# Kernel optimization log

Hardware: AMD Instinct MI355X
Metric: run time of the kernel (lower is better)

Reference implementation:

```python
import jax, jax.numpy as jnp
import numpy as np

B, C, H, W = 16, 512, 32, 32
HID = 4 * C


def setup_inputs() -> dict:
    key = jax.random.key(0)
    k_x, k_w1, k_w2 = jax.random.split(key, 3)
    x = jax.random.normal(k_x, (B, C, H, W), dtype=jnp.float32)
    # 1x1 conv weights stored as [out, in] matrices (kernel_size=1)
    w1 = jax.random.normal(k_w1, (HID, C), dtype=jnp.float32) * (1.0 / np.sqrt(C))
    b1 = jnp.zeros((HID,), dtype=jnp.float32)
    w2 = jax.random.normal(k_w2, (C, HID), dtype=jnp.float32) * (1.0 / np.sqrt(HID))
    b2 = jnp.zeros((C,), dtype=jnp.float32)
    return {"x": x, "w1": w1, "b1": b1, "w2": w2, "b2": b2}


def reference(x, w1, b1, w2, b2):
    Bd, Cd, Hd, Wd = x.shape
    scale = Cd ** (-0.5)
    xf = x.reshape(Bd, Cd, Hd * Wd)          # [B, C, N]
    q = jnp.swapaxes(xf, -1, -2)              # [B, N, C]
    # full spatial self-attention: scores [B, N, N]
    attn = jax.nn.softmax(jnp.einsum('bnc,bcm->bnm', q, xf) * scale, axis=-1)
    out = jnp.einsum('bnm,bmc->bnc', attn, q)  # [B, N, C]
    # 1x1-conv FFN applied per spatial position
    h = jax.nn.relu(jnp.einsum('bnc,dc->bnd', out, w1) + b1)   # [B, N, 4C]
    y = jnp.einsum('bnd,cd->bnc', h, w2) + b2                  # [B, N, C]
    y = jnp.swapaxes(y, -1, -2).reshape(Bd, Cd, Hd, Wd)
    return y + x
```

## Files before the change

kernel.cpp:

```cpp
#include <hip/hip_runtime.h>

#define BATCH 16
#define CH    512
#define NSP   1024
#define HIDD  2048

typedef __bf16 bf16x8 __attribute__((ext_vector_type(8)));
typedef float floatx4 __attribute__((ext_vector_type(4)));

__device__ __forceinline__ float bf2f(unsigned short u) {
    union { unsigned int i; float f; } v; v.i = ((unsigned int)u) << 16; return v.f;
}
__device__ __forceinline__ unsigned short f2bf(float f) {
    union { float f; unsigned int i; } v; v.f = f;
    unsigned int i = v.i;
    return (unsigned short)((i + 0x7FFFu + ((i >> 16) & 1u)) >> 16);
}

__device__ __forceinline__ void gload16(const void* g, void* l) {
    __builtin_amdgcn_global_load_lds(
        (__attribute__((address_space(1))) unsigned int*)(g),
        (__attribute__((address_space(3))) unsigned int*)(l),
        16, 0, 0);
}
#define MEMFENCE asm volatile("" ::: "memory")

template<int EPI, int MAP, int DEPTH>
__global__ __launch_bounds__(256, (DEPTH == 2) ? 3 : 2)
void gemm_bt(const unsigned short* __restrict__ A,
             const unsigned short* __restrict__ Bm,
             void* __restrict__ Cout,
             int Nn, int K,
             long sAb, long sBb, long sCb,
             const float* __restrict__ bias, float scale,
             const float* __restrict__ resid,
             float* __restrict__ aux)
{
    constexpr int NBUF = DEPTH + 1;
    __shared__ unsigned short sA[NBUF][128 * 32];
    __shared__ unsigned short sB[NBUF][128 * 32];
    __shared__ float sInv[128];

    const int tid  = threadIdx.x;
    const int lane = tid & 63;
    const int w    = tid >> 6;
    const int quad = lane >> 4;
    const int l15  = lane & 15;
    const int mw   = (w >> 1) * 64;
    const int nw   = (w & 1) * 64;

    const int F = blockIdx.x;
    int m0, n0, b;
    if constexpr (MAP == 1) {
        const int xcd = F & 7, s = F >> 3;
        b = xcd + ((s >> 5) << 3);
        const int j = s & 31; m0 = (j >> 2) << 7; n0 = (j & 3) << 7;
    } else if constexpr (MAP == 3) {
        const int xcd = F & 7, s = F >> 3;
        b = 0; m0 = (s & 3) << 7; n0 = ((xcd << 4) + (s >> 2)) << 7;
    } else {
        const int xcd = F & 7; int s = F >> 3;
        b = xcd + ((s >= 36) ? 8 : 0);
        if (s >= 36) s -= 36;
        int tm = 0;
        while (s >= 8 - tm) { s -= 8 - tm; tm++; }
        m0 = tm << 7; n0 = (tm + s) << 7;
    }

    if constexpr (EPI == 6) {
        if (tid < 128) {
            const float* p = aux + (size_t)b * NSP * 16
                           + (size_t)(m0 + tid) * 16;
            float s = 0.f;
#pragma unroll
            for (int k = 0; k < 16; k++) s += p[k];
            sInv[tid] = 1.0f / s;
        }
        MEMFENCE;
    }

    A  += (size_t)b * sAb;
    Bm += (size_t)b * sBb;

    const int srow = lane >> 2;
    const int sg   = (lane & 3) ^ ((lane >> 3) & 3);
    const unsigned short* pA = A  + (size_t)(m0 + w * 32 + srow) * K + sg * 8;
    const unsigned short* pB = Bm + (size_t)(n0 + w * 32 + srow) * K + sg * 8;
    const size_t rowskip16 = (size_t)16 * K;
    const int woff = w * 1024;
    const int rslot = ((l15 >> 1) & 3);

    floatx4 acc[4][4];
#pragma unroll
    for (int i = 0; i < 4; i++)
#pragma unroll
        for (int j = 0; j < 4; j++) acc[i][j] = (floatx4){0.f, 0.f, 0.f, 0.f};

    const int nIter = K >> 5;
    const int kLast = K - 32;

#pragma unroll
    for (int d = 0; d < DEPTH; ++d) {
        unsigned short* dA = &sA[d][0] + woff;
        unsigned short* dB = &sB[d][0] + woff;
        gload16(pA + d * 32,             dA);
        gload16(pA + d * 32 + rowskip16, dA + 512);
        gload16(pB + d * 32,             dB);
        gload16(pB + d * 32 + rowskip16, dB + 512);
        MEMFENCE;
    }

    int bcur = 0, bpf = DEPTH;
    for (int it = 0; it < nIter; ++it) {
        if constexpr (DEPTH == 2)
            asm volatile("s_waitcnt vmcnt(4)\n\ts_barrier" ::: "memory");
        else
            asm volatile("s_waitcnt vmcnt(8)\n\ts_barrier" ::: "memory");

        const int kpf = (it + DEPTH) * 32 <= kLast ? (it + DEPTH) * 32 : kLast;
        unsigned short* dA = &sA[0][0] + bpf * 4096 + woff;
        unsigned short* dB = &sB[0][0] + bpf * 4096 + woff;
        gload16(pA + kpf,             dA);
        gload16(pA + kpf + rowskip16, dA + 512);
        gload16(pB + kpf,             dB);
        gload16(pB + kpf + rowskip16, dB + 512);
        MEMFENCE;

        const unsigned short* bufA = &sA[0][0] + bcur * 4096;
        const unsigned short* bufB = &sB[0][0] + bcur * 4096;
        bf16x8 af[4], bfr[4];
#pragma unroll
        for (int mi = 0; mi < 4; mi++)
            af[mi] = *(const bf16x8*)(bufA + (mw + mi * 16 + l15) * 32
                                      + (quad ^ rslot) * 8);
#pragma unroll
        for (int ni = 0; ni < 4; ni++)
            bfr[ni] = *(const bf16x8*)(bufB + (nw + ni * 16 + l15) * 32
                                       + (quad ^ rslot) * 8);
#pragma unroll
        for (int mi = 0; mi < 4; mi++)
#pragma unroll
            for (int ni = 0; ni < 4; ni++)
                acc[mi][ni] = __builtin_amdgcn_mfma_f32_16x16x32_bf16(
                    af[mi], bfr[ni], acc[mi][ni], 0, 0, 0);

        bcur = bcur == NBUF - 1 ? 0 : bcur + 1;
        bpf  = bpf  == NBUF - 1 ? 0 : bpf  + 1;
    }
    asm volatile("s_waitcnt vmcnt(0)" ::: "memory");

    if constexpr (EPI == 4) {
        float* Of = (float*)Cout;
#pragma unroll
        for (int mi = 0; mi < 4; mi++) {
#pragma unroll
            for (int r = 0; r < 4; r++) {
                const int c = m0 + mw + mi * 16 + quad * 4 + r;
                const float bv = bias[c];
#pragma unroll
                for (int ni = 0; ni < 4; ni++) {
                    const int j  = n0 + nw + ni * 16 + l15;
                    const int bb = j >> 10, ns = j & 1023;
                    const size_t a = (size_t)bb * CH * NSP + (size_t)c * NSP + ns;
                    Of[a] = acc[mi][ni][r] + bv + resid[a];
                }
            }
        }
    } else if constexpr (EPI == 5) {
#pragma unroll
        for (int mi = 0; mi < 4; mi++)
#pragma unroll
            for (int ni = 0; ni < 4; ni++)
#pragma unroll
                for (int r = 0; r < 4; r++)
                    acc[mi][ni][r] = __expf(acc[mi][ni][r] * scale);
        {
            const int chunk = (n0 + nw) >> 6;
            float* ps = aux + (size_t)b * NSP * 16;
#pragma unroll
            for (int mi = 0; mi < 4; mi++) {
#pragma unroll
                for (int r = 0; r < 4; r++) {
                    float s = acc[mi][0][r] + acc[mi][1][r]
                            + acc[mi][2][r] + acc[mi][3][r];
                    s += __shfl_xor(s, 1);
                    s += __shfl_xor(s, 2);
                    s += __shfl_xor(s, 4);
                    s += __shfl_xor(s, 8);
                    if (l15 == 0)
                        ps[(size_t)(m0 + mw + mi * 16 + quad * 4 + r) * 16
                           + chunk] = s;
                }
            }
        }
        unsigned short* Cb = (unsigned short*)Cout + (size_t)b * sCb;
#pragma unroll
        for (int mi = 0; mi < 4; mi++) {
#pragma unroll
            for (int r = 0; r < 4; r++) {
                const size_t rowoff =
                    (size_t)(m0 + mw + mi * 16 + quad * 4 + r) * Nn;
#pragma unroll
                for (int ni = 0; ni < 4; ni++)
                    Cb[rowoff + n0 + nw + ni * 16 + l15] =
                        f2bf(acc[mi][ni][r]);
            }
        }
        if constexpr (MAP == 4) {
            if (m0 != n0) {
                const int chunkt = (m0 + mw) >> 6;
                float* ps = aux + (size_t)b * NSP * 16;
#pragma unroll
                for (int ni = 0; ni < 4; ni++) {
                    float s = 0.f;
#pragma unroll
                    for (int mi = 0; mi < 4; mi++)
#pragma unroll
                        for (int r = 0; r < 4; r++) s += acc[mi][ni][r];
                    s += __shfl_xor(s, 16);
                    s += __shfl_xor(s, 32);
                    if (quad == 0)
                        ps[(size_t)(n0 + nw + ni * 16 + l15) * 16 + chunkt] = s;
                }
#pragma unroll
                for (int ni = 0; ni < 4; ni++) {
                    const size_t rowoff =
                        (size_t)(n0 + nw + ni * 16 + l15) * Nn;
#pragma unroll
                    for (int mi = 0; mi < 4; mi++) {
                        ushort4 v;
                        v.x = f2bf(acc[mi][ni][0]);
                        v.y = f2bf(acc[mi][ni][1]);
                        v.z = f2bf(acc[mi][ni][2]);
                        v.w = f2bf(acc[mi][ni][3]);
                        *(ushort4*)(Cb + rowoff + m0 + mw + mi * 16 + quad * 4)
                            = v;
                    }
                }
            }
        }
    } else {
        __syncthreads();
        unsigned short* Cb = (unsigned short*)Cout + (size_t)b * sCb;
#pragma unroll
        for (int mi = 0; mi < 4; mi++) {
#pragma unroll
            for (int r = 0; r < 4; r++) {
                const int lrow = mw + mi * 16 + quad * 4 + r;
                const float iv = sInv[lrow];
                const size_t rowoff = (size_t)(m0 + lrow) * Nn;
#pragma unroll
                for (int ni = 0; ni < 4; ni++)
                    Cb[rowoff + n0 + nw + ni * 16 + l15] =
                        f2bf(acc[mi][ni][r] * iv);
            }
        }
    }
}

__global__ __launch_bounds__(256, 2)
void gemm_final_u2(const unsigned short* __restrict__ A,
                   const unsigned short* __restrict__ Bm,
                   float* __restrict__ Of,
                   const float* __restrict__ bias,
                   const float* __restrict__ resid)
{
    const int K = HIDD;
    __shared__ unsigned short sA[4][128 * 32];
    __shared__ unsigned short sB[4][128 * 32];

    const int tid  = threadIdx.x;
    const int lane = tid & 63;
    const int w    = tid >> 6;
    const int quad = lane >> 4;
    const int l15  = lane & 15;
    const int mw   = (w >> 1) * 64;
    const int nw   = (w & 1) * 64;

    const int F = blockIdx.x;
    const int xcd = F & 7, s = F >> 3;
    const int m0 = (s & 3) << 7;
    const int n0 = ((xcd << 4) + (s >> 2)) << 7;

    const int srow = lane >> 2;
    const int sg   = (lane & 3) ^ ((lane >> 3) & 3);
    const unsigned short* pA = A  + (size_t)(m0 + w * 32 + srow) * K + sg * 8;
    const unsigned short* pB = Bm + (size_t)(n0 + w * 32 + srow) * K + sg * 8;
    const size_t rowskip16 = (size_t)16 * K;
    const int woff = w * 1024;
    const int rslot = ((l15 >> 1) & 3);

    floatx4 acc[4][4];
#pragma unroll
    for (int i = 0; i < 4; i++)
#pragma unroll
        for (int j = 0; j < 4; j++) acc[i][j] = (floatx4){0.f, 0.f, 0.f, 0.f};

    const int kLast = K - 32;

#pragma unroll
    for (int d = 0; d < 4; ++d) {
        unsigned short* dA = &sA[d][0] + woff;
        unsigned short* dB = &sB[d][0] + woff;
        gload16(pA + d * 32,             dA);
        gload16(pA + d * 32 + rowskip16, dA + 512);
        gload16(pB + d * 32,             dB);
        gload16(pB + d * 32 + rowskip16, dB + 512);
        MEMFENCE;
    }

    const int nBody = K >> 6;
    for (int i = 0; i < nBody; ++i) {
        asm volatile("s_waitcnt vmcnt(8)\n\ts_barrier" ::: "memory");

#pragma unroll
        for (int t = 0; t < 2; ++t) {
            const int buf = (2 * i + t) & 3;
            const unsigned short* bufA = &sA[buf][0];
            const unsigned short* bufB = &sB[buf][0];
            bf16x8 af[4], bfr[4];
#pragma unroll
            for (int mi = 0; mi < 4; mi++)
                af[mi] = *(const bf16x8*)(bufA + (mw + mi * 16 + l15) * 32
                                          + (quad ^ rslot) * 8);
#pragma unroll
            for (int ni = 0; ni < 4; ni++)
                bfr[ni] = *(const bf16x8*)(bufB + (nw + ni * 16 + l15) * 32
                                           + (quad ^ rslot) * 8);
#pragma unroll
            for (int mi = 0; mi < 4; mi++)
#pragma unroll
                for (int ni = 0; ni < 4; ni++)
                    acc[mi][ni] = __builtin_amdgcn_mfma_f32_16x16x32_bf16(
                        af[mi], bfr[ni], acc[mi][ni], 0, 0, 0);
        }

        __builtin_amdgcn_s_barrier();
#pragma unroll
        for (int t = 0; t < 2; ++t) {
            const int kt = 2 * i + 4 + t;
            const int kpf = (kt * 32 <= kLast) ? kt * 32 : kLast;
            const int buf = kt & 3;
            unsigned short* dA = &sA[buf][0] + woff;
            unsigned short* dB = &sB[buf][0] + woff;
            gload16(pA + kpf,             dA);
            gload16(pA + kpf + rowskip16, dA + 512);
            gload16(pB + kpf,             dB);
            gload16(pB + kpf + rowskip16, dB + 512);
            MEMFENCE;
        }
    }
    asm volatile("s_waitcnt vmcnt(0)" ::: "memory");

#pragma unroll
    for (int mi = 0; mi < 4; mi++) {
#pragma unroll
        for (int r = 0; r < 4; r++) {
            const int c = m0 + mw + mi * 16 + quad * 4 + r;
            const float bv = bias[c];
#pragma unroll
            for (int ni = 0; ni < 4; ni++) {
                const int j  = n0 + nw + ni * 16 + l15;
                const int bb = j >> 10, ns = j & 1023;
                const size_t a = (size_t)bb * CH * NSP + (size_t)c * NSP + ns;
                Of[a] = acc[mi][ni][r] + bv + resid[a];
            }
        }
    }
}

__global__ __launch_bounds__(256, 3)
void ffn1_wide(const unsigned short* __restrict__ A,
               const unsigned short* __restrict__ Bm,
               unsigned short* __restrict__ Cout,
               const float* __restrict__ bias)
{
    const int K = CH, Nn = HIDD;
    __shared__ unsigned short sA[2][128 * 32];
    __shared__ unsigned short sB[2][256 * 32];

    const int tid  = threadIdx.x;
    const int lane = tid & 63;
    const int w    = tid >> 6;
    const int quad = lane >> 4;
    const int l15  = lane & 15;
    const int mw   = (w >> 1) * 64;
    const int nw   = (w & 1) * 128;

    const int F = blockIdx.x;
    const int xcd = F & 7, s = F >> 3;
    const int m0 = ((xcd << 4) + (s >> 3)) << 7;
    const int n0 = (s & 7) << 8;

    const int srow = lane >> 2;
    const int sg   = (lane & 3) ^ ((lane >> 3) & 3);
    const unsigned short* pA = A  + (size_t)(m0 + w * 32 + srow) * K + sg * 8;
    const unsigned short* pB = Bm + (size_t)(n0 + w * 64 + srow) * K + sg * 8;
    const size_t rowskip16 = (size_t)16 * K;
    const int woffA = w * 1024;
    const int woffB = w * 2048;
    const int rslot = ((l15 >> 1) & 3);

    floatx4 acc[4][8];
#pragma unroll
    for (int i = 0; i < 4; i++)
#pragma unroll
        for (int j = 0; j < 8; j++) acc[i][j] = (floatx4){0.f, 0.f, 0.f, 0.f};

    const int nIter = K >> 5;
    const int kLast = K - 32;

#pragma unroll
    for (int d = 0; d < 2; ++d) {
        unsigned short* dA = &sA[d][0] + woffA;
        unsigned short* dB = &sB[d][0] + woffB;
        gload16(pA + d * 32,                 dA);
        gload16(pA + d * 32 +     rowskip16, dA + 512);
        gload16(pB + d * 32,                 dB);
        gload16(pB + d * 32 +     rowskip16, dB + 512);
        gload16(pB + d * 32 + 2 * rowskip16, dB + 1024);
        gload16(pB + d * 32 + 3 * rowskip16, dB + 1536);
        MEMFENCE;
    }

    for (int it = 0; it < nIter; ++it) {
        asm volatile("s_waitcnt vmcnt(6)\n\ts_barrier" ::: "memory");

        const int cur = it & 1;
        const unsigned short* bufA = &sA[cur][0];
        const unsigned short* bufB = &sB[cur][0];
        bf16x8 af[4], bfr[8];
#pragma unroll
        for (int mi = 0; mi < 4; mi++)
            af[mi] = *(const bf16x8*)(bufA + (mw + mi * 16 + l15) * 32
                                      + (quad ^ rslot) * 8);
#pragma unroll
        for (int ni = 0; ni < 8; ni++)
            bfr[ni] = *(const bf16x8*)(bufB + (nw + ni * 16 + l15) * 32
                                       + (quad ^ rslot) * 8);
#pragma unroll
        for (int mi = 0; mi < 4; mi++)
#pragma unroll
            for (int ni = 0; ni < 8; ni++)
                acc[mi][ni] = __builtin_amdgcn_mfma_f32_16x16x32_bf16(
                    af[mi], bfr[ni], acc[mi][ni], 0, 0, 0);

        __builtin_amdgcn_s_barrier();
        const int kpf = (it + 2) * 32 <= kLast ? (it + 2) * 32 : kLast;
        unsigned short* dA = &sA[cur][0] + woffA;
        unsigned short* dB = &sB[cur][0] + woffB;
        gload16(pA + kpf,                 dA);
        gload16(pA + kpf +     rowskip16, dA + 512);
        gload16(pB + kpf,                 dB);
        gload16(pB + kpf +     rowskip16, dB + 512);
        gload16(pB + kpf + 2 * rowskip16, dB + 1024);
        gload16(pB + kpf + 3 * rowskip16, dB + 1536);
        MEMFENCE;
    }
    asm volatile("s_waitcnt vmcnt(0)" ::: "memory");

    float bv[8];
#pragma unroll
    for (int ni = 0; ni < 8; ni++) bv[ni] = bias[n0 + nw + ni * 16 + l15];
#pragma unroll
    for (int mi = 0; mi < 4; mi++) {
#pragma unroll
        for (int r = 0; r < 4; r++) {
            const size_t rowoff =
                (size_t)(m0 + mw + mi * 16 + quad * 4 + r) * Nn;
#pragma unroll
            for (int ni = 0; ni < 8; ni++)
                Cout[rowoff + n0 + nw + ni * 16 + l15] =
                    f2bf(fmaxf(acc[mi][ni][r] + bv[ni], 0.f));
        }
    }
}

__global__ __launch_bounds__(256)
void prep_kernel(const float* __restrict__ x,
                 unsigned short* __restrict__ Xbf,
                 unsigned short* __restrict__ XT,
                 const float* __restrict__ w1,
                 unsigned short* __restrict__ W1b,
                 const float* __restrict__ w2,
                 unsigned short* __restrict__ W2b)
{
    const int tx = threadIdx.x, ty = threadIdx.y;
    const int z = blockIdx.z;
    if (z < 16) {
        __shared__ float tile[32][33];
        const int n0 = blockIdx.x * 32, c0 = blockIdx.y * 32, b = z;
        const size_t base = (size_t)b * CH * NSP;
#pragma unroll
        for (int i = ty; i < 32; i += 8) {
            float v = x[base + (size_t)(c0 + i) * NSP + n0 + tx];
            tile[i][tx] = v;
            Xbf[base + (size_t)(c0 + i) * NSP + n0 + tx] = f2bf(v);
        }
        __syncthreads();
        const size_t tbase = (size_t)b * NSP * CH;
#pragma unroll
        for (int i = ty; i < 32; i += 8)
            XT[tbase + (size_t)(n0 + i) * CH + c0 + tx] = f2bf(tile[tx][i]);
    } else {
        const int tid = ty * 32 + tx;
        const int blk = (z - 16) * 512 + blockIdx.y * 32 + blockIdx.x;
        const int i = blk * 256 + tid;
        if (i < HIDD * CH) W1b[i] = f2bf(w1[i]);
        else               W2b[i - HIDD * CH] = f2bf(w2[i - HIDD * CH]);
    }
}

extern "C" void kernel_launch(void* const* d_in, const int* in_sizes, int n_in,
                              void* d_out, int out_size, void* d_ws, size_t ws_size,
                              hipStream_t stream)
{
    const float* x  = (const float*)d_in[0];
    const float* w1 = (const float*)d_in[1];
    const float* b1 = (const float*)d_in[2];
    const float* w2 = (const float*)d_in[3];
    const float* b2 = (const float*)d_in[4];
    float* out = (float*)d_out;

    char* ws = (char*)d_ws;
    unsigned short* Xbf = (unsigned short*)ws; ws += (size_t)BATCH * CH * NSP * 2;
    unsigned short* XT  = (unsigned short*)ws; ws += (size_t)BATCH * NSP * CH * 2;
    unsigned short* W1b = (unsigned short*)ws; ws += (size_t)HIDD * CH * 2;
    unsigned short* W2b = (unsigned short*)ws; ws += (size_t)CH * HIDD * 2;
    unsigned short* P   = (unsigned short*)ws; ws += (size_t)BATCH * NSP * NSP * 2;
    unsigned short* O   = (unsigned short*)ws; ws += (size_t)BATCH * NSP * CH * 2;
    unsigned short* Hb  = (unsigned short*)ws; ws += (size_t)BATCH * NSP * HIDD * 2;
    float*          Ps  = (float*)ws;          ws += (size_t)BATCH * NSP * 16 * 4;

    const dim3 blk(256);

    prep_kernel<<<dim3(32, 16, 32), dim3(32, 8), 0, stream>>>(
        x, Xbf, XT, w1, W1b, w2, W2b);

    gemm_bt<5, 4, 2><<<dim3(576), blk, 0, stream>>>(
        XT, XT, P, NSP, CH,
        (long)NSP * CH, (long)NSP * CH, (long)NSP * NSP, nullptr,
        0.04419417382415922f, nullptr, Ps);

    gemm_bt<6, 1, 2><<<dim3(512), blk, 0, stream>>>(
        P, Xbf, O, CH, NSP,
        (long)NSP * NSP, (long)CH * NSP, (long)NSP * CH, nullptr, 1.f,
        nullptr, Ps);

    ffn1_wide<<<dim3(1024), blk, 0, stream>>>(O, W1b, Hb, b1);

    gemm_final_u2<<<dim3(512), blk, 0, stream>>>(
        W2b, Hb, out, b2, x);
}
```

Before: 262.6 us.

## Rewrite FFN1 GEMM as 256x256 tile, 8-wave phased pipeline kernel

```diff
diff --git a/kernel.cpp b/kernel.cpp
--- a/kernel.cpp
+++ b/kernel.cpp
@@ -24,6 +24,7 @@
         16, 0, 0);
 }
 #define MEMFENCE asm volatile("" ::: "memory")
+#define SBARRIER asm volatile("s_barrier" ::: "memory")
 
 template<int EPI, int MAP, int DEPTH>
 __global__ __launch_bounds__(256, (DEPTH == 2) ? 3 : 2)
@@ -369,111 +370,171 @@
     }
 }
 
-__global__ __launch_bounds__(256, 3)
-void ffn1_wide(const unsigned short* __restrict__ A,
-               const unsigned short* __restrict__ Bm,
-               unsigned short* __restrict__ Cout,
-               const float* __restrict__ bias)
+__global__ __launch_bounds__(512, 1)
+void ffn1_8ph(const unsigned short* __restrict__ A,
+              const unsigned short* __restrict__ Bm,
+              unsigned short* __restrict__ Cout,
+              const float* __restrict__ bias)
 {
-    const int K = CH, Nn = HIDD;
-    __shared__ unsigned short sA[2][128 * 32];
-    __shared__ unsigned short sB[2][256 * 32];
+    constexpr int K = CH;
+    __shared__ unsigned short sA[2][256 * 64];
+    __shared__ unsigned short sB[2][256 * 64];
 
     const int tid  = threadIdx.x;
     const int lane = tid & 63;
     const int w    = tid >> 6;
+    const int wr   = w >> 2;
+    const int wc   = w & 3;
     const int quad = lane >> 4;
     const int l15  = lane & 15;
-    const int mw   = (w >> 1) * 64;
-    const int nw   = (w & 1) * 128;
+    const int swz  = (l15 & 4) ? 16 : 0;
 
     const int F = blockIdx.x;
     const int xcd = F & 7, s = F >> 3;
-    const int m0 = ((xcd << 4) + (s >> 3)) << 7;
+    const int m0 = ((xcd << 3) + (s >> 3)) << 8;
     const int n0 = (s & 7) << 8;
 
-    const int srow = lane >> 2;
-    const int sg   = (lane & 3) ^ ((lane >> 3) & 3);
-    const unsigned short* pA = A  + (size_t)(m0 + w * 32 + srow) * K + sg * 8;
-    const unsigned short* pB = Bm + (size_t)(n0 + w * 64 + srow) * K + sg * 8;
-    const size_t rowskip16 = (size_t)16 * K;
-    const int woffA = w * 1024;
-    const int woffB = w * 2048;
-    const int rslot = ((l15 >> 1) & 3);
-
-    floatx4 acc[4][8];
-#pragma unroll
-    for (int i = 0; i < 4; i++)
-#pragma unroll
-        for (int j = 0; j < 8; j++) acc[i][j] = (floatx4){0.f, 0.f, 0.f, 0.f};
-
-    const int nIter = K >> 5;
-    const int kLast = K - 32;
-
-#pragma unroll
-    for (int d = 0; d < 2; ++d) {
-        unsigned short* dA = &sA[d][0] + woffA;
-        unsigned short* dB = &sB[d][0] + woffB;
-        gload16(pA + d * 32,                 dA);
-        gload16(pA + d * 32 +     rowskip16, dA + 512);
-        gload16(pB + d * 32,                 dB);
-        gload16(pB + d * 32 +     rowskip16, dB + 512);
-        gload16(pB + d * 32 + 2 * rowskip16, dB + 1024);
-        gload16(pB + d * 32 + 3 * rowskip16, dB + 1536);
-        MEMFENCE;
-    }
-
-    for (int it = 0; it < nIter; ++it) {
-        asm volatile("s_waitcnt vmcnt(6)\n\ts_barrier" ::: "memory");
-
-        const int cur = it & 1;
-        const unsigned short* bufA = &sA[cur][0];
-        const unsigned short* bufB = &sB[cur][0];
-        bf16x8 af[4], bfr[8];
-#pragma unroll
-        for (int mi = 0; mi < 4; mi++)
-            af[mi] = *(const bf16x8*)(bufA + (mw + mi * 16 + l15) * 32
-                                      + (quad ^ rslot) * 8);
-#pragma unroll
-        for (int ni = 0; ni < 8; ni++)
-            bfr[ni] = *(const bf16x8*)(bufB + (nw + ni * 16 + l15) * 32
-                                       + (quad ^ rslot) * 8);
-#pragma unroll
-        for (int mi = 0; mi < 4; mi++)
-#pragma unroll
-            for (int ni = 0; ni < 8; ni++)
-                acc[mi][ni] = __builtin_amdgcn_mfma_f32_16x16x32_bf16(
-                    af[mi], bfr[ni], acc[mi][ni], 0, 0, 0);
-
-        __builtin_amdgcn_s_barrier();
-        const int kpf = (it + 2) * 32 <= kLast ? (it + 2) * 32 : kLast;
-        unsigned short* dA = &sA[cur][0] + woffA;
-        unsigned short* dB = &sB[cur][0] + woffB;
-        gload16(pA + kpf,                 dA);
-        gload16(pA + kpf +     rowskip16, dA + 512);
-        gload16(pB + kpf,                 dB);
-        gload16(pB + kpf +     rowskip16, dB + 512);
-        gload16(pB + kpf + 2 * rowskip16, dB + 1024);
-        gload16(pB + kpf + 3 * rowskip16, dB + 1536);
-        MEMFENCE;
-    }
+    const int srow   = tid >> 3;
+    const int schunk = (tid & 7) ^ ((tid & 32) >> 4);
+    const unsigned short* pAg = A  + (size_t)(m0 + srow) * K + schunk * 8;
+    const unsigned short* pBg = Bm + (size_t)(n0 + srow) * K + schunk * 8;
+    const int dRow = w * 8;
+
+#define STAGE_A8(kt, nb) do {                                         \
+    unsigned short* d = &sA[nb][0];                                   \
+    const unsigned short* g = pAg + (kt) * 64;                        \
+    gload16(g,                   d + (dRow      ) * 64);              \
+    gload16(g + (size_t) 64 * K, d + (dRow +  64) * 64);              \
+    gload16(g + (size_t)128 * K, d + (dRow + 128) * 64);              \
+    gload16(g + (size_t)192 * K, d + (dRow + 192) * 64);              \
+    MEMFENCE; } while (0)
+#define STAGE_B8(kt, nb) do {                                         \
+    unsigned short* d = &sB[nb][0];                                   \
+    const unsigned short* g = pBg + (kt) * 64;                        \
+    gload16(g,                   d + (dRow      ) * 64);              \
+    gload16(g + (size_t) 64 * K, d + (dRow +  64) * 64);              \
+    gload16(g + (size_t)128 * K, d + (dRow + 128) * 64);              \
+    gload16(g + (size_t)192 * K, d + (dRow + 192) * 64);              \
+    MEMFENCE; } while (0)
+
+    floatx4 acc[8][4];
+#pragma unroll
+    for (int i = 0; i < 8; i++)
+#pragma unroll
+        for (int j = 0; j < 4; j++) acc[i][j] = (floatx4){0.f, 0.f, 0.f, 0.f};
+
+    STAGE_A8(0, 0);
+    STAGE_B8(0, 0);
     asm volatile("s_waitcnt vmcnt(0)" ::: "memory");
-
-    float bv[8];
-#pragma unroll
-    for (int ni = 0; ni < 8; ni++) bv[ni] = bias[n0 + nw + ni * 16 + l15];
-#pragma unroll
-    for (int mi = 0; mi < 4; mi++) {
+    SBARRIER;
+
+    bf16x8 af[4][2], bfr[4][2];
+
+    for (int kt = 0; kt < 8; ++kt) {
+        const unsigned short* bufA = &sA[kt & 1][0];
+        const unsigned short* bufB = &sB[kt & 1][0];
+        const int nb = (kt + 1) & 1;
+        const bool pf = (kt < 7);
+
+#pragma unroll
+        for (int i = 0; i < 4; i++) {
+            const unsigned short* r = bufA + (size_t)(wr * 128 + i * 16 + l15) * 64;
+            af[i][0] = *(const bf16x8*)(r + ((quad * 8) ^ swz));
+            af[i][1] = *(const bf16x8*)(r + ((32 + quad * 8) ^ swz));
+        }
+#pragma unroll
+        for (int j = 0; j < 2; j++) {
+            const unsigned short* r = bufB + (size_t)(wc * 64 + j * 16 + l15) * 64;
+            bfr[j][0] = *(const bf16x8*)(r + ((quad * 8) ^ swz));
+            bfr[j][1] = *(const bf16x8*)(r + ((32 + quad * 8) ^ swz));
+        }
+        if (pf) STAGE_A8(kt + 1, nb);
+        SBARRIER;
+        __builtin_amdgcn_s_setprio(1);
+#pragma unroll
+        for (int i = 0; i < 4; i++)
+#pragma unroll
+            for (int j = 0; j < 2; j++)
+#pragma unroll
+                for (int kk = 0; kk < 2; kk++)
+                    acc[i][j] = __builtin_amdgcn_mfma_f32_16x16x32_bf16(
+                        af[i][kk], bfr[j][kk], acc[i][j], 0, 0, 0);
+        __builtin_amdgcn_s_setprio(0);
+        SBARRIER;
+
+#pragma unroll
+        for (int j = 0; j < 2; j++) {
+            const unsigned short* r = bufB + (size_t)(wc * 64 + (2 + j) * 16 + l15) * 64;
+            bfr[2 + j][0] = *(const bf16x8*)(r + ((quad * 8) ^ swz));
+            bfr[2 + j][1] = *(const bf16x8*)(r + ((32 + quad * 8) ^ swz));
+        }
+        if (pf) STAGE_B8(kt + 1, nb);
+        SBARRIER;
+        __builtin_amdgcn_s_setprio(1);
+#pragma unroll
+        for (int i = 0; i < 4; i++)
+#pragma unroll
+            for (int j = 0; j < 2; j++)
+#pragma unroll
+                for (int kk = 0; kk < 2; kk++)
+                    acc[i][2 + j] = __builtin_amdgcn_mfma_f32_16x16x32_bf16(
+                        af[i][kk], bfr[2 + j][kk], acc[i][2 + j], 0, 0, 0);
+        __builtin_amdgcn_s_setprio(0);
+        SBARRIER;
+
+#pragma unroll
+        for (int i = 0; i < 4; i++) {
+            const unsigned short* r = bufA + (size_t)(wr * 128 + 64 + i * 16 + l15) * 64;
+            af[i][0] = *(const bf16x8*)(r + ((quad * 8) ^ swz));
+            af[i][1] = *(const bf16x8*)(r + ((32 + quad * 8) ^ swz));
+        }
+        SBARRIER;
+        __builtin_amdgcn_s_setprio(1);
+#pragma unroll
+        for (int i = 0; i < 4; i++)
+#pragma unroll
+            for (int j = 0; j < 2; j++)
+#pragma unroll
+                for (int kk = 0; kk < 2; kk++)
+                    acc[4 + i][2 + j] = __builtin_amdgcn_mfma_f32_16x16x32_bf16(
+                        af[i][kk], bfr[2 + j][kk], acc[4 + i][2 + j], 0, 0, 0);
+        __builtin_amdgcn_s_setprio(0);
+        SBARRIER;
+
+        __builtin_amdgcn_s_setprio(1);
+#pragma unroll
+        for (int i = 0; i < 4; i++)
+#pragma unroll
+            for (int j = 0; j < 2; j++)
+#pragma unroll
+                for (int kk = 0; kk < 2; kk++)
+                    acc[4 + i][j] = __builtin_amdgcn_mfma_f32_16x16x32_bf16(
+                        af[i][kk], bfr[j][kk], acc[4 + i][j], 0, 0, 0);
+        __builtin_amdgcn_s_setprio(0);
+        if (pf) {
+            asm volatile("s_waitcnt vmcnt(0)" ::: "memory");
+            SBARRIER;
+        }
+    }
+
+    float bv[4];
+#pragma unroll
+    for (int ni = 0; ni < 4; ni++)
+        bv[ni] = bias[n0 + wc * 64 + ni * 16 + l15];
+#pragma unroll
+    for (int mi = 0; mi < 8; mi++) {
 #pragma unroll
         for (int r = 0; r < 4; r++) {
             const size_t rowoff =
-                (size_t)(m0 + mw + mi * 16 + quad * 4 + r) * Nn;
-#pragma unroll
-            for (int ni = 0; ni < 8; ni++)
-                Cout[rowoff + n0 + nw + ni * 16 + l15] =
+                (size_t)(m0 + wr * 128 + mi * 16 + quad * 4 + r) * HIDD;
+#pragma unroll
+            for (int ni = 0; ni < 4; ni++)
+                Cout[rowoff + n0 + wc * 64 + ni * 16 + l15] =
                     f2bf(fmaxf(acc[mi][ni][r] + bv[ni], 0.f));
         }
     }
+#undef STAGE_A8
+#undef STAGE_B8
 }
 
 __global__ __launch_bounds__(256)
@@ -547,7 +608,7 @@
         (long)NSP * NSP, (long)CH * NSP, (long)NSP * CH, nullptr, 1.f,
         nullptr, Ps);
 
-    ffn1_wide<<<dim3(1024), blk, 0, stream>>>(O, W1b, Hb, b1);
+    ffn1_8ph<<<dim3(512), dim3(512), 0, stream>>>(O, W1b, Hb, b1);
 
     gemm_final_u2<<<dim3(512), blk, 0, stream>>>(
         W2b, Hb, out, b2, x);
```

Measured after the change: 237.4 us. -9.6%, faster.
